# Optimization experiments

Measured on AMD Instinct MI355X. Metric: run time of the kernel, lower is better.

Reference implementation:

```python
import jax, jax.numpy as jnp
import numpy as np

B, N, F = 512, 2048, 64
T = 4            # number of atom types
H1, H2 = 64, 32  # hidden widths; final layer outputs 1 (per-atom energy)


def setup_inputs() -> dict:
    key = jax.random.key(0)
    ks = jax.random.split(key, 8)
    x = jax.random.normal(ks[0], (B, N, F), dtype=jnp.float32)
    atomic_numbers = jax.random.randint(ks[1], (N,), 0, T)
    s = 0.05
    # Per-type MLP parameters, stacked over the type axis (torch Linear layout: [out, in]).
    w0 = jax.random.normal(ks[2], (T, H1, F), dtype=jnp.float32) * s
    b0 = jax.random.normal(ks[3], (T, H1), dtype=jnp.float32) * s
    w1 = jax.random.normal(ks[4], (T, H2, H1), dtype=jnp.float32) * s
    b1 = jax.random.normal(ks[5], (T, H2), dtype=jnp.float32) * s
    w2 = jax.random.normal(ks[6], (T, 1, H2), dtype=jnp.float32) * s
    b2 = jax.random.normal(ks[7], (T, 1), dtype=jnp.float32) * s
    return {"x": x, "atomic_numbers": atomic_numbers,
            "w0": w0, "b0": b0, "w1": w1, "b1": b1, "w2": w2, "b2": b2}


def reference(x, atomic_numbers, w0, b0, w1, b1, w2, b2):
    # Behler-Parrinello: route each atom through the MLP of its atom type,
    # then sum per-atom energies over atoms.  The torch version gathers atoms
    # by type, runs each type's MLP, and scatters back; here we evaluate all
    # T type-MLPs batched over the type axis and select with a one-hot mask
    # (identical math, jit-friendly, no data-dependent shapes).
    onehot = jax.nn.one_hot(atomic_numbers, w0.shape[0], dtype=x.dtype)  # [N, T]
    h = jax.nn.silu(jnp.einsum('bnf,thf->tbnh', x, w0) + b0[:, None, None, :])   # [T,B,N,H1]
    h = jax.nn.silu(jnp.einsum('tbnh,tgh->tbng', h, w1) + b1[:, None, None, :])  # [T,B,N,H2]
    e = jnp.einsum('tbng,tog->tbno', h, w2) + b2[:, None, None, :]               # [T,B,N,1]
    e = e[..., 0]                                                                # [T,B,N]
    per_atom = jnp.einsum('tbn,nt->bn', e, onehot)  # select the matching type per atom
    return per_atom.sum(axis=-1)                    # [B]
```

## Files before the change

kernel.cpp:

```cpp
#include <hip/hip_runtime.h>
#include <hip/hip_bf16.h>


#define B_ 512
#define N_ 2048
#define F_ 64
#define T_ 4
#define H1_ 64
#define H2_ 32

#define BT 16
#define WAVES 4
#define NCHUNK 64
#define SLICE (NCHUNK / WAVES)

typedef __attribute__((ext_vector_type(8))) short bf16x8;
typedef __attribute__((ext_vector_type(4))) short bf16x4;
typedef __attribute__((ext_vector_type(4))) float f32x4;

__device__ inline float silu_f(float v) {
    return v * __builtin_amdgcn_rcpf(1.0f + __expf(-v));
}

__device__ inline bf16x8 pack8(float4 a, float4 b) {
    union { __hip_bfloat162 h[4]; bf16x8 v; } u;
    u.h[0] = __float22bfloat162_rn({a.x, a.y});
    u.h[1] = __float22bfloat162_rn({a.z, a.w});
    u.h[2] = __float22bfloat162_rn({b.x, b.y});
    u.h[3] = __float22bfloat162_rn({b.z, b.w});
    return u.v;
}

__device__ inline bf16x4 pack4(float a, float b, float c, float d) {
    union { __hip_bfloat162 h[2]; bf16x4 v; } u;
    u.h[0] = __float22bfloat162_rn({a, b});
    u.h[1] = __float22bfloat162_rn({c, d});
    return u.v;
}

__device__ inline float bf_at(bf16x4 v, int r) {
    union { bf16x4 v; __hip_bfloat16 h[4]; } u; u.v = v;
    return __bfloat162float(u.h[r]);
}

__global__ void sort_atoms(const int* __restrict__ an, int* __restrict__ sorted) {
    const int lane = threadIdx.x;
    int v[32];
#pragma unroll
    for (int c = 0; c < 32; ++c) v[c] = an[c * 64 + lane];

    int c0 = 0, c1 = 0, c2 = 0;
#pragma unroll
    for (int c = 0; c < 32; ++c) {
        c0 += __popcll(__ballot(v[c] == 0));
        c1 += __popcll(__ballot(v[c] == 1));
        c2 += __popcll(__ballot(v[c] == 2));
    }
    int base0 = 0, base1 = c0, base2 = c0 + c1, base3 = c0 + c1 + c2;
    const unsigned long long mb = (1ull << lane) - 1ull;
#pragma unroll
    for (int c = 0; c < 32; ++c) {
        const int t = v[c];
        unsigned long long m0 = __ballot(t == 0);
        unsigned long long m1 = __ballot(t == 1);
        unsigned long long m2 = __ballot(t == 2);
        unsigned long long m3 = __ballot(t == 3);
        int pos;
        if (t == 0)      pos = base0 + (int)__popcll(m0 & mb);
        else if (t == 1) pos = base1 + (int)__popcll(m1 & mb);
        else if (t == 2) pos = base2 + (int)__popcll(m2 & mb);
        else             pos = base3 + (int)__popcll(m3 & mb);
        sorted[pos] = (t << 16) | (c * 64 + lane);
        base0 += (int)__popcll(m0); base1 += (int)__popcll(m1);
        base2 += (int)__popcll(m2); base3 += (int)__popcll(m3);
    }
}

__global__ __launch_bounds__(256, 3) void bpnn_kernel(
    const float* __restrict__ x, const int* __restrict__ sorted,
    const float* __restrict__ w0, const float* __restrict__ b0,
    const float* __restrict__ w1, const float* __restrict__ b1,
    const float* __restrict__ w2, const float* __restrict__ b2,
    float* __restrict__ out)
{
    __shared__ __align__(16) __hip_bfloat16 trb[WAVES][BT][68];
    __shared__ float red[BT];

    const int tid  = threadIdx.x;
    const int wave = tid >> 6;
    const int lane = tid & 63;
    const int lr   = lane & 15;
    const int q    = lane >> 4;
    const int b0i  = blockIdx.y * BT;

    if (tid < BT) red[tid] = 0.0f;
    __syncthreads();

    const float* xb_ = x + (size_t)(b0i + lr) * (N_ * F_) + q * 8;
    __hip_bfloat16* trbw = &trb[wave][lr][0];

    const int s0 = blockIdx.x * NCHUNK + wave * SLICE;
    const int s1 = s0 + SLICE;

    float esum0 = 0.f, esum1 = 0.f, bsum = 0.f;

    bf16x8 aw000, aw001, aw010, aw011, aw020, aw021, aw030, aw031;
    bf16x8 aw100, aw101, aw110, aw111;
    bf16x4 b0f0, b0f1, b0f2, b0f3, b1f0, b1f1, w2f0, w2f1;
    float b2c = 0.f;

    int p = s0;
    int id0 = __builtin_amdgcn_readfirstlane(sorted[p]);
    int id1 = __builtin_amdgcn_readfirstlane(sorted[p + 1]);
    float4 sa0, sa1, sa2, sa3, sb0, sb1, sb2, sb3;
    {
        const float4* pA = reinterpret_cast<const float4*>(xb_ + (id0 & 0xFFFF) * F_);
        sa0 = pA[0]; sa1 = pA[1]; sa2 = pA[8]; sa3 = pA[9];
        const float4* pB = reinterpret_cast<const float4*>(xb_ + (id1 & 0xFFFF) * F_);
        sb0 = pB[0]; sb1 = pB[1]; sb2 = pB[8]; sb3 = pB[9];
    }

    while (p < s1) {
        const int t = id0 >> 16;
        {
            const float* wb = w0 + t * (H1_ * F_) + lr * F_ + q * 8;
            const float4* pw;
            pw = reinterpret_cast<const float4*>(wb +  0 * F_ +  0); aw000 = pack8(pw[0], pw[1]);
            pw = reinterpret_cast<const float4*>(wb +  0 * F_ + 32); aw001 = pack8(pw[0], pw[1]);
            pw = reinterpret_cast<const float4*>(wb + 16 * F_ +  0); aw010 = pack8(pw[0], pw[1]);
            pw = reinterpret_cast<const float4*>(wb + 16 * F_ + 32); aw011 = pack8(pw[0], pw[1]);
            pw = reinterpret_cast<const float4*>(wb + 32 * F_ +  0); aw020 = pack8(pw[0], pw[1]);
            pw = reinterpret_cast<const float4*>(wb + 32 * F_ + 32); aw021 = pack8(pw[0], pw[1]);
            pw = reinterpret_cast<const float4*>(wb + 48 * F_ +  0); aw030 = pack8(pw[0], pw[1]);
            pw = reinterpret_cast<const float4*>(wb + 48 * F_ + 32); aw031 = pack8(pw[0], pw[1]);
            const float* wc = w1 + t * (H2_ * H1_) + lr * H1_ + q * 8;
            pw = reinterpret_cast<const float4*>(wc +  0 * H1_ +  0); aw100 = pack8(pw[0], pw[1]);
            pw = reinterpret_cast<const float4*>(wc +  0 * H1_ + 32); aw101 = pack8(pw[0], pw[1]);
            pw = reinterpret_cast<const float4*>(wc + 16 * H1_ +  0); aw110 = pack8(pw[0], pw[1]);
            pw = reinterpret_cast<const float4*>(wc + 16 * H1_ + 32); aw111 = pack8(pw[0], pw[1]);
            float4 v;
            v = *reinterpret_cast<const float4*>(b0 + t * H1_ +  0 + q * 4); b0f0 = pack4(v.x, v.y, v.z, v.w);
            v = *reinterpret_cast<const float4*>(b0 + t * H1_ + 16 + q * 4); b0f1 = pack4(v.x, v.y, v.z, v.w);
            v = *reinterpret_cast<const float4*>(b0 + t * H1_ + 32 + q * 4); b0f2 = pack4(v.x, v.y, v.z, v.w);
            v = *reinterpret_cast<const float4*>(b0 + t * H1_ + 48 + q * 4); b0f3 = pack4(v.x, v.y, v.z, v.w);
            v = *reinterpret_cast<const float4*>(b1 + t * H2_ +  0 + q * 4); b1f0 = pack4(v.x, v.y, v.z, v.w);
            v = *reinterpret_cast<const float4*>(b1 + t * H2_ + 16 + q * 4); b1f1 = pack4(v.x, v.y, v.z, v.w);
            v = *reinterpret_cast<const float4*>(w2 + t * H2_ +  0 + q * 4); w2f0 = pack4(v.x, v.y, v.z, v.w);
            v = *reinterpret_cast<const float4*>(w2 + t * H2_ + 16 + q * 4); w2f1 = pack4(v.x, v.y, v.z, v.w);
            b2c = b2[t];
        }

        for (;;) {
            bf16x8 xf0 = pack8(sa0, sa1);
            bf16x8 xf1 = pack8(sa2, sa3);
            sa0 = sb0; sa1 = sb1; sa2 = sb2; sa3 = sb3;
            int pn = p + 2;
            int idn = id1;
            if (pn < s1) idn = __builtin_amdgcn_readfirstlane(sorted[pn]);
            {
                const float4* pB = reinterpret_cast<const float4*>(xb_ + (idn & 0xFFFF) * F_);
                sb0 = pB[0]; sb1 = pB[1]; sb2 = pB[8]; sb3 = pB[9];
            }
            bsum += b2c;

            f32x4 acc0 = {0.f,0.f,0.f,0.f}, acc1 = {0.f,0.f,0.f,0.f};
            f32x4 acc2 = {0.f,0.f,0.f,0.f}, acc3 = {0.f,0.f,0.f,0.f};
            acc0 = __builtin_amdgcn_mfma_f32_16x16x32_bf16(aw000, xf0, acc0, 0, 0, 0);
            acc0 = __builtin_amdgcn_mfma_f32_16x16x32_bf16(aw001, xf1, acc0, 0, 0, 0);
            acc1 = __builtin_amdgcn_mfma_f32_16x16x32_bf16(aw010, xf0, acc1, 0, 0, 0);
            acc1 = __builtin_amdgcn_mfma_f32_16x16x32_bf16(aw011, xf1, acc1, 0, 0, 0);
            acc2 = __builtin_amdgcn_mfma_f32_16x16x32_bf16(aw020, xf0, acc2, 0, 0, 0);
            acc2 = __builtin_amdgcn_mfma_f32_16x16x32_bf16(aw021, xf1, acc2, 0, 0, 0);
            acc3 = __builtin_amdgcn_mfma_f32_16x16x32_bf16(aw030, xf0, acc3, 0, 0, 0);
            acc3 = __builtin_amdgcn_mfma_f32_16x16x32_bf16(aw031, xf1, acc3, 0, 0, 0);

            {
                float v0 = silu_f(acc0[0] + bf_at(b0f0, 0));
                float v1 = silu_f(acc0[1] + bf_at(b0f0, 1));
                float v2 = silu_f(acc0[2] + bf_at(b0f0, 2));
                float v3 = silu_f(acc0[3] + bf_at(b0f0, 3));
                *reinterpret_cast<bf16x4*>(trbw +  0 + q * 4) = pack4(v0, v1, v2, v3);
                v0 = silu_f(acc1[0] + bf_at(b0f1, 0));
                v1 = silu_f(acc1[1] + bf_at(b0f1, 1));
                v2 = silu_f(acc1[2] + bf_at(b0f1, 2));
                v3 = silu_f(acc1[3] + bf_at(b0f1, 3));
                *reinterpret_cast<bf16x4*>(trbw + 16 + q * 4) = pack4(v0, v1, v2, v3);
                v0 = silu_f(acc2[0] + bf_at(b0f2, 0));
                v1 = silu_f(acc2[1] + bf_at(b0f2, 1));
                v2 = silu_f(acc2[2] + bf_at(b0f2, 2));
                v3 = silu_f(acc2[3] + bf_at(b0f2, 3));
                *reinterpret_cast<bf16x4*>(trbw + 32 + q * 4) = pack4(v0, v1, v2, v3);
                v0 = silu_f(acc3[0] + bf_at(b0f3, 0));
                v1 = silu_f(acc3[1] + bf_at(b0f3, 1));
                v2 = silu_f(acc3[2] + bf_at(b0f3, 2));
                v3 = silu_f(acc3[3] + bf_at(b0f3, 3));
                *reinterpret_cast<bf16x4*>(trbw + 48 + q * 4) = pack4(v0, v1, v2, v3);
            }
            __builtin_amdgcn_wave_barrier();

            bf16x8 hb0 = *reinterpret_cast<const bf16x8*>(trbw + q * 8);
            bf16x8 hb1 = *reinterpret_cast<const bf16x8*>(trbw + 32 + q * 8);
            __builtin_amdgcn_wave_barrier();

            f32x4 acB0 = {0.f,0.f,0.f,0.f}, acB1 = {0.f,0.f,0.f,0.f};
            acB0 = __builtin_amdgcn_mfma_f32_16x16x32_bf16(aw100, hb0, acB0, 0, 0, 0);
            acB0 = __builtin_amdgcn_mfma_f32_16x16x32_bf16(aw101, hb1, acB0, 0, 0, 0);
            acB1 = __builtin_amdgcn_mfma_f32_16x16x32_bf16(aw110, hb0, acB1, 0, 0, 0);
            acB1 = __builtin_amdgcn_mfma_f32_16x16x32_bf16(aw111, hb1, acB1, 0, 0, 0);

#pragma unroll
            for (int r = 0; r < 4; ++r) {
                esum0 += silu_f(acB0[r] + bf_at(b1f0, r)) * bf_at(w2f0, r);
                esum1 += silu_f(acB1[r] + bf_at(b1f1, r)) * bf_at(w2f1, r);
            }

            ++p;
            id0 = id1; id1 = idn;
            if (p >= s1 || (id0 >> 16) != t) break;
        }
    }

    float esum = esum0 + esum1;
    esum += __shfl_xor(esum, 16);
    esum += __shfl_xor(esum, 32);
    if (q == 0) atomicAdd(&red[lr], esum + bsum);
    __syncthreads();
    if (tid < BT) atomicAdd(&out[b0i + tid], red[tid]);
}

extern "C" void kernel_launch(void* const* d_in, const int* in_sizes, int n_in,
                              void* d_out, int out_size, void* d_ws, size_t ws_size,
                              hipStream_t stream) {
    const float* x  = (const float*)d_in[0];
    const int*   an = (const int*)d_in[1];
    const float* w0 = (const float*)d_in[2];
    const float* b0 = (const float*)d_in[3];
    const float* w1 = (const float*)d_in[4];
    const float* b1 = (const float*)d_in[5];
    const float* w2 = (const float*)d_in[6];
    const float* b2 = (const float*)d_in[7];
    float* out = (float*)d_out;
    int* sorted = (int*)d_ws;

    hipMemsetAsync(out, 0, B_ * sizeof(float), stream);
    sort_atoms<<<1, 64, 0, stream>>>(an, sorted);
    dim3 grid(N_ / NCHUNK, B_ / BT);
    bpnn_kernel<<<grid, 256, 0, stream>>>(x, sorted, w0, b0, w1, b1, w2, b2, out);
}
```

Before: 397.5 us.

## Use single-wave blocks with register-held atom ids and fold output zeroing into sort

Each block shrinks from four waves to one wave covering 16 sorted atoms. The wave loads the chunk's atom ids once into a register and broadcasts them with readlane, replacing per-iteration scalar loads from global memory. The LDS reduction and block barriers go away, and every wave atomically adds straight into the output. The memset is folded into the sort kernel, which removes one launch. In exchange the grid has four times more blocks, and there are more global atomics and more weight reloads per block.

```diff
diff --git a/kernel.cpp b/kernel.cpp
--- a/kernel.cpp
+++ b/kernel.cpp
@@ -10,9 +10,7 @@
 #define H2_ 32
 
 #define BT 16
-#define WAVES 4
-#define NCHUNK 64
-#define SLICE (NCHUNK / WAVES)
+#define NCHUNK 16
 
 typedef __attribute__((ext_vector_type(8))) short bf16x8;
 typedef __attribute__((ext_vector_type(4))) short bf16x4;
@@ -43,8 +41,12 @@
     return __bfloat162float(u.h[r]);
 }
 
-__global__ void sort_atoms(const int* __restrict__ an, int* __restrict__ sorted) {
+__global__ void sort_atoms(const int* __restrict__ an, int* __restrict__ sorted,
+                           float* __restrict__ out) {
     const int lane = threadIdx.x;
+#pragma unroll
+    for (int i = 0; i < B_ / 64; ++i) out[i * 64 + lane] = 0.0f;
+
     int v[32];
 #pragma unroll
     for (int c = 0; c < 32; ++c) v[c] = an[c * 64 + lane];
@@ -76,31 +78,26 @@
     }
 }
 
-__global__ __launch_bounds__(256, 3) void bpnn_kernel(
+__global__ __launch_bounds__(64, 3) void bpnn_kernel(
     const float* __restrict__ x, const int* __restrict__ sorted,
     const float* __restrict__ w0, const float* __restrict__ b0,
     const float* __restrict__ w1, const float* __restrict__ b1,
     const float* __restrict__ w2, const float* __restrict__ b2,
     float* __restrict__ out)
 {
-    __shared__ __align__(16) __hip_bfloat16 trb[WAVES][BT][68];
-    __shared__ float red[BT];
-
-    const int tid  = threadIdx.x;
-    const int wave = tid >> 6;
-    const int lane = tid & 63;
+    __shared__ __align__(16) __hip_bfloat16 trb[BT][68];
+
+    const int lane = threadIdx.x;
     const int lr   = lane & 15;
     const int q    = lane >> 4;
     const int b0i  = blockIdx.y * BT;
-
-    if (tid < BT) red[tid] = 0.0f;
-    __syncthreads();
+    const int s0   = blockIdx.x * NCHUNK;
+
+    int myid = 0;
+    if (lane < NCHUNK) myid = sorted[s0 + lane];
 
     const float* xb_ = x + (size_t)(b0i + lr) * (N_ * F_) + q * 8;
-    __hip_bfloat16* trbw = &trb[wave][lr][0];
-
-    const int s0 = blockIdx.x * NCHUNK + wave * SLICE;
-    const int s1 = s0 + SLICE;
+    __hip_bfloat16* trbw = &trb[lr][0];
 
     float esum0 = 0.f, esum1 = 0.f, bsum = 0.f;
 
@@ -109,18 +106,18 @@
     bf16x4 b0f0, b0f1, b0f2, b0f3, b1f0, b1f1, w2f0, w2f1;
     float b2c = 0.f;
 
-    int p = s0;
-    int id0 = __builtin_amdgcn_readfirstlane(sorted[p]);
-    int id1 = __builtin_amdgcn_readfirstlane(sorted[p + 1]);
+    int i = 0;
+    int id0 = __builtin_amdgcn_readlane(myid, 0);
+    int id1 = __builtin_amdgcn_readlane(myid, 1);
     float4 sa0, sa1, sa2, sa3, sb0, sb1, sb2, sb3;
     {
-        const float4* pA = reinterpret_cast<const float4*>(xb_ + (id0 & 0xFFFF) * F_);
+        const float4* pA = reinterpret_cast<const float4*>(xb_ + (size_t)(id0 & 0xFFFF) * F_);
         sa0 = pA[0]; sa1 = pA[1]; sa2 = pA[8]; sa3 = pA[9];
-        const float4* pB = reinterpret_cast<const float4*>(xb_ + (id1 & 0xFFFF) * F_);
+        const float4* pB = reinterpret_cast<const float4*>(xb_ + (size_t)(id1 & 0xFFFF) * F_);
         sb0 = pB[0]; sb1 = pB[1]; sb2 = pB[8]; sb3 = pB[9];
     }
 
-    while (p < s1) {
+    while (i < NCHUNK) {
         const int t = id0 >> 16;
         {
             const float* wb = w0 + t * (H1_ * F_) + lr * F_ + q * 8;
@@ -154,11 +151,10 @@
             bf16x8 xf0 = pack8(sa0, sa1);
             bf16x8 xf1 = pack8(sa2, sa3);
             sa0 = sb0; sa1 = sb1; sa2 = sb2; sa3 = sb3;
-            int pn = p + 2;
-            int idn = id1;
-            if (pn < s1) idn = __builtin_amdgcn_readfirstlane(sorted[pn]);
+            int in2 = (i + 2 < NCHUNK) ? i + 2 : NCHUNK - 1;
+            int idn = __builtin_amdgcn_readlane(myid, in2);
             {
-                const float4* pB = reinterpret_cast<const float4*>(xb_ + (idn & 0xFFFF) * F_);
+                const float4* pB = reinterpret_cast<const float4*>(xb_ + (size_t)(idn & 0xFFFF) * F_);
                 sb0 = pB[0]; sb1 = pB[1]; sb2 = pB[8]; sb3 = pB[9];
             }
             bsum += b2c;
@@ -214,18 +210,16 @@
                 esum1 += silu_f(acB1[r] + bf_at(b1f1, r)) * bf_at(w2f1, r);
             }
 
-            ++p;
+            ++i;
             id0 = id1; id1 = idn;
-            if (p >= s1 || (id0 >> 16) != t) break;
+            if (i >= NCHUNK || (id0 >> 16) != t) break;
         }
     }
 
     float esum = esum0 + esum1;
     esum += __shfl_xor(esum, 16);
     esum += __shfl_xor(esum, 32);
-    if (q == 0) atomicAdd(&red[lr], esum + bsum);
-    __syncthreads();
-    if (tid < BT) atomicAdd(&out[b0i + tid], red[tid]);
+    if (q == 0) atomicAdd(&out[b0i + lr], esum + bsum);
 }
 
 extern "C" void kernel_launch(void* const* d_in, const int* in_sizes, int n_in,
@@ -242,8 +236,7 @@
     float* out = (float*)d_out;
     int* sorted = (int*)d_ws;
 
-    hipMemsetAsync(out, 0, B_ * sizeof(float), stream);
-    sort_atoms<<<1, 64, 0, stream>>>(an, sorted);
+    sort_atoms<<<1, 64, 0, stream>>>(an, sorted, out);
     dim3 grid(N_ / NCHUNK, B_ / BT);
-    bpnn_kernel<<<grid, 256, 0, stream>>>(x, sorted, w0, b0, w1, b1, w2, b2, out);
-}
+    bpnn_kernel<<<grid, 64, 0, stream>>>(x, sorted, w0, b0, w1, b1, w2, b2, out);
+}
```

Result: no change. 393.1 us (-1.1%).
